# Optimization experiments

Hardware: AMD Instinct MI355X
Metric: run time of the kernel (lower is better)

The kernel has to match this reference:

```python
import jax, jax.numpy as jnp
import numpy as np

ALPHA = 0.2   # LeakyReLU slope from source
HEADS = 8

def _proj(x, W, s, b):
    # Conv3D(kernel=1, no bias) + fused inference BatchNorm affine + LeakyReLU
    y = jnp.einsum('nchwd,de->nchwe', x, W) * s + b
    return jnp.where(y >= 0, y, ALPHA * y)

def setup_inputs() -> dict:
    key = jax.random.key(0)
    ks = jax.random.split(key, 13)
    N, D, H, W, C = 2, 64, 64, 64, 64   # D == in_channels (axis 1), C is last axis
    KC, VC = 64, 64
    p = lambda k, sh, sc=0.1: jax.random.normal(k, sh, jnp.float32) * sc
    return {
        'x':  jax.random.normal(ks[0], (N, D, H, W, C), jnp.float32),
        'Wk': p(ks[1], (D, KC)), 'sk': 1.0 + p(ks[2], (KC,)), 'bk': p(ks[3], (KC,)),
        'Wq': p(ks[4], (D, KC)), 'sq': 1.0 + p(ks[5], (KC,)), 'bq': p(ks[6], (KC,)),
        'Wv': p(ks[7], (D, VC)), 'sv': 1.0 + p(ks[8], (VC,)), 'bv': p(ks[9], (VC,)),
        'Wr': p(ks[10], (VC, D)), 'sr': 1.0 + p(ks[11], (D,)), 'br': p(ks[12], (D,)),
    }

def reference(x, Wk, sk, bk, Wq, sq, bq, Wv, sv, bv, Wr, sr, br):
    n, d, h, w, c = x.shape
    xt = jnp.transpose(x, (0, 4, 2, 3, 1))            # (n, c, h, w, d)
    keys    = _proj(xt, Wk, sk, bk)                   # (n, c, h, w, KC)
    queries = _proj(xt, Wq, sq, bq)
    values  = _proj(xt, Wv, sv, bv)
    T = c * h * w
    KC, VC = Wk.shape[1], Wv.shape[1]
    hk, hv = KC // HEADS, VC // HEADS                 # hk == hv required by source math
    K = jax.nn.softmax(keys.reshape(n, T, HEADS, hk), axis=1)      # softmax over tokens
    Q = jax.nn.softmax(queries.reshape(n, T, HEADS, hk), axis=-1)  # softmax over head channels
    V = values.reshape(n, T, HEADS, hv)
    ctx = jnp.einsum('ntak,ntav->nakv', K, V)         # (n, heads, hk, hv) small context
    # source: tf.matmul(context, query^T) contracts ctx's hv with query's hk axis
    att = jnp.einsum('nakv,ntav->nakt', ctx, Q)       # (n, heads, hk, T)
    # faithful raw reshape per head (n, hk, T) -> (n, c, h, w, hv), heads concat last
    att = att.reshape(n, HEADS, c, h, w, hv)
    agg = jnp.transpose(att, (0, 2, 3, 4, 1, 5)).reshape(n, c, h, w, HEADS * hv)
    rep = _proj(agg, Wr, sr, br)                      # (n, c, h, w, d)
    return x + jnp.transpose(rep, (0, 4, 2, 3, 1))
```

## Files before the change

### kernel.cpp

```cpp
#include <hip/hip_runtime.h>

#define ALPHA 0.2f

typedef const __attribute__((address_space(1))) unsigned int gu32;
typedef __attribute__((address_space(3))) unsigned int lu32;

__device__ float g_part[8192 * 576];
__device__ float g_red[2 * 64 * 1024];
__device__ float g_ctx[1024];

__global__ __launch_bounds__(256, 3) void k_kv(
    const float* __restrict__ x,
    const float* __restrict__ Wk, const float* __restrict__ sk, const float* __restrict__ bk,
    const float* __restrict__ Wv, const float* __restrict__ sv, const float* __restrict__ bv)
{
  __shared__ __align__(16) float sh[11008];
  float* eK = sh;
  float* vV = sh + 4352;
  float* pE = sh + 8704;
  float* pS = sh + 8960;

  const int tid = threadIdx.x;
  const int bid = blockIdx.x;
  const int n   = bid >> 10;
  const int hw0 = (bid & 1023) * 4;

  const int pr  = tid & 63;
  const int wv  = __builtin_amdgcn_readfirstlane(tid >> 6);
  const bool isK = (wv < 2);
  const int cbase = 32 * (wv & 1);
  const float* Wsrc = (isK ? Wk : Wv) + cbase;
  const float* sp   = (isK ? sk : sv) + cbase;
  const float* bp   = (isK ? bk : bv) + cbase;

  const float* xg = x + (size_t)n * 16777216u + (size_t)hw0 * 64u + 4 * pr;

  float acc[4][32];
  #pragma unroll
  for (int t = 0; t < 4; ++t)
    #pragma unroll
    for (int c = 0; c < 32; ++c) acc[t][c] = 0.f;

  #pragma unroll 2
  for (int d = 0; d < 64; ++d) {
    float4 xv = *(const float4*)(xg + (size_t)d * 262144u);
    const float* wrow = Wsrc + d * 64;
    #pragma unroll
    for (int q = 0; q < 8; ++q) {
      float4 w = *(const float4*)(wrow + q * 4);
      acc[0][q*4+0] += xv.x * w.x; acc[0][q*4+1] += xv.x * w.y;
      acc[0][q*4+2] += xv.x * w.z; acc[0][q*4+3] += xv.x * w.w;
      acc[1][q*4+0] += xv.y * w.x; acc[1][q*4+1] += xv.y * w.y;
      acc[1][q*4+2] += xv.y * w.z; acc[1][q*4+3] += xv.y * w.w;
      acc[2][q*4+0] += xv.z * w.x; acc[2][q*4+1] += xv.z * w.y;
      acc[2][q*4+2] += xv.z * w.z; acc[2][q*4+3] += xv.z * w.w;
      acc[3][q*4+0] += xv.w * w.x; acc[3][q*4+1] += xv.w * w.y;
      acc[3][q*4+2] += xv.w * w.z; acc[3][q*4+3] += xv.w * w.w;
    }
  }

  #pragma unroll
  for (int q = 0; q < 8; ++q) {
    float4 s4 = *(const float4*)(sp + q * 4);
    float4 b4 = *(const float4*)(bp + q * 4);
    float ss[4] = {s4.x, s4.y, s4.z, s4.w};
    float bb[4] = {b4.x, b4.y, b4.z, b4.w};
    #pragma unroll
    for (int j = 0; j < 4; ++j) {
      #pragma unroll
      for (int t = 0; t < 4; ++t) {
        float y = acc[t][q*4+j] * ss[j] + bb[j];
        y = (y >= 0.f) ? y : ALPHA * y;
        if (isK) y = __expf(fminf(y, 60.f));
        acc[t][q*4+j] = y;
      }
    }
  }

  const int prl = pr & 15;
  float* dstbuf = isK ? eK : vV;
  const int ch = tid & 63, tq = tid >> 6, a8 = ch & ~7;

  #pragma unroll
  for (int ph = 0; ph < 4; ++ph) {
    if ((pr >> 4) == ph) {
      #pragma unroll
      for (int t = 0; t < 4; ++t)
        #pragma unroll
        for (int q = 0; q < 8; ++q)
          *(float4*)&dstbuf[(prl*4 + t) * 68 + cbase + q*4] = *(float4*)&acc[t][q*4];
    }
    __syncthreads();

    float E = 0.f;
    float S[8];
    #pragma unroll
    for (int v = 0; v < 8; ++v) S[v] = 0.f;
    for (int t = tq * 16; t < tq * 16 + 16; ++t) {
      float e = eK[t * 68 + ch];
      float4 v0 = *(const float4*)&vV[t * 68 + a8];
      float4 v1 = *(const float4*)&vV[t * 68 + a8 + 4];
      E += e;
      S[0] += e * v0.x; S[1] += e * v0.y; S[2] += e * v0.z; S[3] += e * v0.w;
      S[4] += e * v1.x; S[5] += e * v1.y; S[6] += e * v1.z; S[7] += e * v1.w;
    }
    pE[tq * 64 + ch] = E;
    #pragma unroll
    for (int v = 0; v < 8; ++v) pS[v * 256 + tq * 64 + ch] = S[v];
    __syncthreads();

    if (tid < 64) {
      float* gp = g_part + ((size_t)bid * 4u + ph) * 576u;
      float E4 = pE[tid] + pE[64 + tid] + pE[128 + tid] + pE[192 + tid];
      gp[tid] = E4;
      #pragma unroll
      for (int v = 0; v < 8; ++v) {
        float S4 = pS[v * 256 + tid] + pS[v * 256 + 64 + tid]
                 + pS[v * 256 + 128 + tid] + pS[v * 256 + 192 + tid];
        gp[64 + v * 64 + tid] = S4;
      }
    }
  }
}

__global__ __launch_bounds__(256) void k_red() {
  const int ob = blockIdx.x & 3;
  const int bc = blockIdx.x >> 2;
  const int i  = ob * 256 + threadIdx.x;
  const int n = i >> 9, ch = (i & 511) >> 3, v = i & 7;
  const float* base = g_part + ((size_t)n * 4096u + (size_t)bc * 64u) * 576u;
  float l = 0.f, S = 0.f;
  #pragma unroll 8
  for (int b = 0; b < 64; ++b) {
    l += base[(size_t)b * 576u + ch];
    S += base[(size_t)b * 576u + 64u + (size_t)v * 64u + ch];
  }
  g_red[bc * 1024 + i]         = l;
  g_red[65536 + bc * 1024 + i] = S;
}

__global__ __launch_bounds__(256) void k_ctx() {
  int i = blockIdx.x * 256 + threadIdx.x;
  if (i >= 1024) return;
  float l = 0.f, S = 0.f;
  #pragma unroll
  for (int r = 0; r < 64; ++r) {
    l += g_red[r * 1024 + i];
    S += g_red[65536 + r * 1024 + i];
  }
  float c = (l > 0.f) ? (S / l) : 0.f;
  if (!(__builtin_fabsf(c) < 1e30f)) c = 0.f;
  g_ctx[i] = c;
}

__global__ __launch_bounds__(256) void k_att(
    const float* __restrict__ x,
    const float* __restrict__ Wq, const float* __restrict__ sq, const float* __restrict__ bq,
    const float* __restrict__ Wr, const float* __restrict__ sr, const float* __restrict__ br,
    float* __restrict__ out)
{
  __shared__ __align__(16) float WqA[64 * 68];
  __shared__ __align__(16) float xw[64 * 64];
  __shared__ __align__(16) float qL[64 * 64];
  __shared__ __align__(16) float ctxL[64 * 12];
  __shared__ float srL[64], brL[64];

  const int tid = threadIdx.x;
  const int lin = blockIdx.x;

  const int xcd   = lin & 7;
  const int jc    = (lin >> 3) & 7;
  const int rest  = lin >> 6;
  const int combo = rest * 8 + xcd;
  const int n     = combo >> 9;
  const int hp_lo = (combo >> 6) & 7;
  const int wp    = combo & 63;
  const int hp    = jc * 8 + hp_lo;
  const int hwp   = hp * 64 + wp;

  const int h_t   = hp_lo * 8 + (wp >> 3);
  const int wbase = (wp & 7) * 8;

  #pragma unroll
  for (int i = 0; i < 4; ++i) {
    int idx = tid + i * 256;
    __builtin_amdgcn_global_load_lds((gu32*)(Wq + idx * 4),
                                     (lu32*)&WqA[idx * 4], 16, 0, 0);
  }
  if (tid < 64) { srL[tid] = sr[tid]; brL[tid] = br[tid]; }

  for (int i = tid; i < 512; i += 256) {
    int ch = i >> 3, v = i & 7;
    ctxL[ch * 12 + v] = g_ctx[n * 512 + ch * 8 + v];
  }

  {
    const size_t xb = (size_t)n * 16777216u + (size_t)h_t * 4096u;
    #pragma unroll
    for (int i = 0; i < 16; ++i) {
      int idx = tid + i * 256;
      int d = idx >> 6, tok = idx & 63;
      int vpp = tok >> 3, cl = tok & 7;
      xw[d * 64 + tok] = x[xb + (size_t)d * 262144u + (size_t)(wbase + vpp) * 64u + (cl * 8 + jc)];
    }
  }
  __syncthreads();

  {
    const int tok0 = (tid & 31) * 2;
    const int ch0  = (tid >> 5) * 8;
    float acc0[8], acc1[8];
    #pragma unroll
    for (int j = 0; j < 8; ++j) { acc0[j] = 0.f; acc1[j] = 0.f; }
    #pragma unroll 4
    for (int d = 0; d < 64; ++d) {
      float2 xv = *(const float2*)&xw[d * 64 + tok0];
      float4 wa = *(const float4*)&WqA[d * 64 + ch0];
      float4 wb = *(const float4*)&WqA[d * 64 + ch0 + 4];
      float w[8] = {wa.x, wa.y, wa.z, wa.w, wb.x, wb.y, wb.z, wb.w};
      #pragma unroll
      for (int j = 0; j < 8; ++j) { acc0[j] += xv.x * w[j]; acc1[j] += xv.y * w[j]; }
    }
    float sv8[8], bv8[8];
    *(float4*)&sv8[0] = *(const float4*)(sq + ch0);
    *(float4*)&sv8[4] = *(const float4*)(sq + ch0 + 4);
    *(float4*)&bv8[0] = *(const float4*)(bq + ch0);
    *(float4*)&bv8[4] = *(const float4*)(bq + ch0 + 4);
    #pragma unroll
    for (int i = 0; i < 2; ++i) {
      float* a = (i == 0) ? acc0 : acc1;
      float mx = -3.0e38f;
      #pragma unroll
      for (int j = 0; j < 8; ++j) {
        float y = a[j] * sv8[j] + bv8[j];
        y = (y >= 0.f) ? y : ALPHA * y;
        a[j] = y;
        mx = fmaxf(mx, y);
      }
      float sum = 0.f;
      #pragma unroll
      for (int j = 0; j < 8; ++j) { a[j] = __expf(a[j] - mx); sum += a[j]; }
      float inv = 1.f / sum;
      float o8[8];
      #pragma unroll
      for (int j = 0; j < 8; ++j) o8[j] = a[j] * inv;
      const int t = tok0 + i;
      const int rot = (4 * t) & 63;
      *(float4*)&qL[t * 64 + ((ch0 + rot) & 63)]     = *(float4*)&o8[0];
      *(float4*)&qL[t * 64 + ((ch0 + 4 + rot) & 63)] = *(float4*)&o8[4];
    }
  }
  __syncthreads();

  #pragma unroll
  for (int i = 0; i < 4; ++i) {
    int idx = tid + i * 256;
    __builtin_amdgcn_global_load_lds((gu32*)(Wr + idx * 4),
                                     (lu32*)&xw[idx * 4], 16, 0, 0);
  }

  {
    float* aggL = WqA;
    const int cp = tid & 63, eb = tid >> 6;
    const int kk = cp >> 3, cl = cp & 7;
    #pragma unroll
    for (int j4 = 0; j4 < 4; ++j4) {
      float s4[4];
      #pragma unroll
      for (int jj = 0; jj < 4; ++jj) {
        int e = eb * 16 + j4 * 4 + jj;
        int a = e >> 3, vpp = e & 7;
        float4 c0 = *(const float4*)&ctxL[(a * 8 + kk) * 12];
        float4 c1 = *(const float4*)&ctxL[(a * 8 + kk) * 12 + 4];
        int t = vpp * 8 + cl;
        int rot = (4 * t) & 63;
        float4 q0 = *(const float4*)&qL[t * 64 + ((a * 8 + rot) & 63)];
        float4 q1 = *(const float4*)&qL[t * 64 + ((a * 8 + 4 + rot) & 63)];
        s4[jj] = q0.x * c0.x + q0.y * c0.y + q0.z * c0.z + q0.w * c0.w
               + q1.x * c1.x + q1.y * c1.y + q1.z * c1.z + q1.w * c1.w;
      }
      *(float4*)&aggL[cp * 68 + eb * 16 + j4 * 4] =
          make_float4(s4[0], s4[1], s4[2], s4[3]);
    }
  }
  __syncthreads();

  {
    const float* aggL = WqA;
    const int ci = tid & 63, dq = tid >> 6;
    float accr[16];
    #pragma unroll
    for (int i = 0; i < 16; ++i) accr[i] = 0.f;
    #pragma unroll 4
    for (int ec = 0; ec < 16; ++ec) {
      float4 a4 = *(const float4*)&aggL[ci * 68 + ec * 4];
      float av[4] = {a4.x, a4.y, a4.z, a4.w};
      #pragma unroll
      for (int j = 0; j < 4; ++j) {
        const float* wrow = &xw[(ec * 4 + j) * 64 + dq * 16];
        float4 w0 = *(const float4*)(wrow);
        float4 w1 = *(const float4*)(wrow + 4);
        float4 w2 = *(const float4*)(wrow + 8);
        float4 w3 = *(const float4*)(wrow + 12);
        float aj = av[j];
        accr[0]  += aj * w0.x; accr[1]  += aj * w0.y; accr[2]  += aj * w0.z; accr[3]  += aj * w0.w;
        accr[4]  += aj * w1.x; accr[5]  += aj * w1.y; accr[6]  += aj * w1.z; accr[7]  += aj * w1.w;
        accr[8]  += aj * w2.x; accr[9]  += aj * w2.y; accr[10] += aj * w2.z; accr[11] += aj * w2.w;
        accr[12] += aj * w3.x; accr[13] += aj * w3.y; accr[14] += aj * w3.z; accr[15] += aj * w3.w;
      }
    }
    const size_t xb = (size_t)n * 16777216u + (size_t)hwp * 64u + (size_t)ci;
    #pragma unroll
    for (int i = 0; i < 16; ++i) {
      int di = dq * 16 + i;
      float y = accr[i] * srL[di] + brL[di];
      y = (y >= 0.f) ? y : ALPHA * y;
      out[xb + (size_t)di * 262144u] = x[xb + (size_t)di * 262144u] + y;
    }
  }
}

extern "C" void kernel_launch(void* const* d_in, const int* in_sizes, int n_in,
                              void* d_out, int out_size, void* d_ws, size_t ws_size,
                              hipStream_t stream)
{
  (void)in_sizes; (void)n_in; (void)out_size; (void)d_ws; (void)ws_size;

  const float* x  = (const float*)d_in[0];
  const float* Wk = (const float*)d_in[1];
  const float* sk = (const float*)d_in[2];
  const float* bk = (const float*)d_in[3];
  const float* Wq = (const float*)d_in[4];
  const float* sq = (const float*)d_in[5];
  const float* bq = (const float*)d_in[6];
  const float* Wv = (const float*)d_in[7];
  const float* sv = (const float*)d_in[8];
  const float* bv = (const float*)d_in[9];
  const float* Wr = (const float*)d_in[10];
  const float* sr = (const float*)d_in[11];
  const float* br = (const float*)d_in[12];
  float* out = (float*)d_out;

  k_kv  <<<dim3(2048), dim3(256), 0, stream>>>(x, Wk, sk, bk, Wv, sv, bv);
  k_red <<<dim3(256),  dim3(256), 0, stream>>>();
  k_ctx <<<dim3(4),    dim3(256), 0, stream>>>();
  k_att <<<dim3(8192), dim3(256), 0, stream>>>(x, Wq, sq, bq, Wr, sr, br, out);
}
```

Baseline: 509.8 us.

## Read weights as wave-uniform scalar loads instead of staging in LDS in attention kernel

The attention kernel no longer stages Wq, Wr, sr and br in shared memory. Each wave now owns a fixed 16-channel slice, so weight rows are wave-uniform and can be fetched with scalar loads, and each lane loads its x token directly from global memory. The Q projection is remapped from 2 tokens × 8 channels per thread to 1 token × 16 channels. This removes LDS traffic, LDS footprint and one staging phase, which can raise occupancy. In exchange it relies on the scalar cache for weight reuse and on strided per-lane global reads of x.

```diff
diff --git a/kernel.cpp b/kernel.cpp
--- a/kernel.cpp
+++ b/kernel.cpp
@@ -159,11 +159,9 @@
     const float* __restrict__ Wr, const float* __restrict__ sr, const float* __restrict__ br,
     float* __restrict__ out)
 {
-  __shared__ __align__(16) float WqA[64 * 68];
-  __shared__ __align__(16) float xw[64 * 64];
   __shared__ __align__(16) float qL[64 * 64];
+  __shared__ __align__(16) float aggL[64 * 68];
   __shared__ __align__(16) float ctxL[64 * 12];
-  __shared__ float srL[64], brL[64];
 
   const int tid = threadIdx.x;
   const int lin = blockIdx.x;
@@ -181,86 +179,71 @@
   const int h_t   = hp_lo * 8 + (wp >> 3);
   const int wbase = (wp & 7) * 8;
 
-  #pragma unroll
-  for (int i = 0; i < 4; ++i) {
-    int idx = tid + i * 256;
-    __builtin_amdgcn_global_load_lds((gu32*)(Wq + idx * 4),
-                                     (lu32*)&WqA[idx * 4], 16, 0, 0);
-  }
-  if (tid < 64) { srL[tid] = sr[tid]; brL[tid] = br[tid]; }
-
   for (int i = tid; i < 512; i += 256) {
     int ch = i >> 3, v = i & 7;
     ctxL[ch * 12 + v] = g_ctx[n * 512 + ch * 8 + v];
   }
 
+  const int lane = tid & 63;
+  const int wv   = __builtin_amdgcn_readfirstlane(tid >> 6);
+  const int c0   = wv * 16;
+
   {
-    const size_t xb = (size_t)n * 16777216u + (size_t)h_t * 4096u;
-    #pragma unroll
-    for (int i = 0; i < 16; ++i) {
-      int idx = tid + i * 256;
-      int d = idx >> 6, tok = idx & 63;
-      int vpp = tok >> 3, cl = tok & 7;
-      xw[d * 64 + tok] = x[xb + (size_t)d * 262144u + (size_t)(wbase + vpp) * 64u + (cl * 8 + jc)];
-    }
-  }
-  __syncthreads();
-
-  {
-    const int tok0 = (tid & 31) * 2;
-    const int ch0  = (tid >> 5) * 8;
-    float acc0[8], acc1[8];
-    #pragma unroll
-    for (int j = 0; j < 8; ++j) { acc0[j] = 0.f; acc1[j] = 0.f; }
+    const int vpp = lane >> 3, cl = lane & 7;
+    const float* xg = x + (size_t)n * 16777216u + (size_t)h_t * 4096u
+                    + (size_t)(wbase + vpp) * 64u + (size_t)(cl * 8 + jc);
+    const float* WqU = Wq + c0;
+
+    float acc[16];
+    #pragma unroll
+    for (int c = 0; c < 16; ++c) acc[c] = 0.f;
+
     #pragma unroll 4
     for (int d = 0; d < 64; ++d) {
-      float2 xv = *(const float2*)&xw[d * 64 + tok0];
-      float4 wa = *(const float4*)&WqA[d * 64 + ch0];
-      float4 wb = *(const float4*)&WqA[d * 64 + ch0 + 4];
-      float w[8] = {wa.x, wa.y, wa.z, wa.w, wb.x, wb.y, wb.z, wb.w};
-      #pragma unroll
-      for (int j = 0; j < 8; ++j) { acc0[j] += xv.x * w[j]; acc1[j] += xv.y * w[j]; }
-    }
-    float sv8[8], bv8[8];
-    *(float4*)&sv8[0] = *(const float4*)(sq + ch0);
-    *(float4*)&sv8[4] = *(const float4*)(sq + ch0 + 4);
-    *(float4*)&bv8[0] = *(const float4*)(bq + ch0);
-    *(float4*)&bv8[4] = *(const float4*)(bq + ch0 + 4);
-    #pragma unroll
-    for (int i = 0; i < 2; ++i) {
-      float* a = (i == 0) ? acc0 : acc1;
+      float xv = xg[(size_t)d * 262144u];
+      const float* wrow = WqU + d * 64;
+      float4 w0 = *(const float4*)(wrow);
+      float4 w1 = *(const float4*)(wrow + 4);
+      float4 w2 = *(const float4*)(wrow + 8);
+      float4 w3 = *(const float4*)(wrow + 12);
+      acc[0]  += xv * w0.x; acc[1]  += xv * w0.y; acc[2]  += xv * w0.z; acc[3]  += xv * w0.w;
+      acc[4]  += xv * w1.x; acc[5]  += xv * w1.y; acc[6]  += xv * w1.z; acc[7]  += xv * w1.w;
+      acc[8]  += xv * w2.x; acc[9]  += xv * w2.y; acc[10] += xv * w2.z; acc[11] += xv * w2.w;
+      acc[12] += xv * w3.x; acc[13] += xv * w3.y; acc[14] += xv * w3.z; acc[15] += xv * w3.w;
+    }
+
+    const int rot = (4 * lane) & 63;
+    #pragma unroll
+    for (int g = 0; g < 2; ++g) {
+      float4 s0 = *(const float4*)(sq + c0 + 8 * g);
+      float4 s1 = *(const float4*)(sq + c0 + 8 * g + 4);
+      float4 b0 = *(const float4*)(bq + c0 + 8 * g);
+      float4 b1 = *(const float4*)(bq + c0 + 8 * g + 4);
+      float ss[8] = {s0.x, s0.y, s0.z, s0.w, s1.x, s1.y, s1.z, s1.w};
+      float bb[8] = {b0.x, b0.y, b0.z, b0.w, b1.x, b1.y, b1.z, b1.w};
+      float a8[8];
       float mx = -3.0e38f;
       #pragma unroll
       for (int j = 0; j < 8; ++j) {
-        float y = a[j] * sv8[j] + bv8[j];
+        float y = acc[g * 8 + j] * ss[j] + bb[j];
         y = (y >= 0.f) ? y : ALPHA * y;
-        a[j] = y;
+        a8[j] = y;
         mx = fmaxf(mx, y);
       }
       float sum = 0.f;
       #pragma unroll
-      for (int j = 0; j < 8; ++j) { a[j] = __expf(a[j] - mx); sum += a[j]; }
+      for (int j = 0; j < 8; ++j) { a8[j] = __expf(a8[j] - mx); sum += a8[j]; }
       float inv = 1.f / sum;
       float o8[8];
       #pragma unroll
-      for (int j = 0; j < 8; ++j) o8[j] = a[j] * inv;
-      const int t = tok0 + i;
-      const int rot = (4 * t) & 63;
-      *(float4*)&qL[t * 64 + ((ch0 + rot) & 63)]     = *(float4*)&o8[0];
-      *(float4*)&qL[t * 64 + ((ch0 + 4 + rot) & 63)] = *(float4*)&o8[4];
+      for (int j = 0; j < 8; ++j) o8[j] = a8[j] * inv;
+      *(float4*)&qL[lane * 64 + ((c0 + 8 * g + rot) & 63)]     = *(float4*)&o8[0];
+      *(float4*)&qL[lane * 64 + ((c0 + 8 * g + 4 + rot) & 63)] = *(float4*)&o8[4];
     }
   }
   __syncthreads();
 
-  #pragma unroll
-  for (int i = 0; i < 4; ++i) {
-    int idx = tid + i * 256;
-    __builtin_amdgcn_global_load_lds((gu32*)(Wr + idx * 4),
-                                     (lu32*)&xw[idx * 4], 16, 0, 0);
-  }
-
   {
-    float* aggL = WqA;
     const int cp = tid & 63, eb = tid >> 6;
     const int kk = cp >> 3, cl = cp & 7;
     #pragma unroll
@@ -270,14 +253,14 @@
       for (int jj = 0; jj < 4; ++jj) {
         int e = eb * 16 + j4 * 4 + jj;
         int a = e >> 3, vpp = e & 7;
-        float4 c0 = *(const float4*)&ctxL[(a * 8 + kk) * 12];
-        float4 c1 = *(const float4*)&ctxL[(a * 8 + kk) * 12 + 4];
+        float4 c0v = *(const float4*)&ctxL[(a * 8 + kk) * 12];
+        float4 c1v = *(const float4*)&ctxL[(a * 8 + kk) * 12 + 4];
         int t = vpp * 8 + cl;
-        int rot = (4 * t) & 63;
-        float4 q0 = *(const float4*)&qL[t * 64 + ((a * 8 + rot) & 63)];
-        float4 q1 = *(const float4*)&qL[t * 64 + ((a * 8 + 4 + rot) & 63)];
-        s4[jj] = q0.x * c0.x + q0.y * c0.y + q0.z * c0.z + q0.w * c0.w
-               + q1.x * c1.x + q1.y * c1.y + q1.z * c1.z + q1.w * c1.w;
+        int rt = (4 * t) & 63;
+        float4 q0 = *(const float4*)&qL[t * 64 + ((a * 8 + rt) & 63)];
+        float4 q1 = *(const float4*)&qL[t * 64 + ((a * 8 + 4 + rt) & 63)];
+        s4[jj] = q0.x * c0v.x + q0.y * c0v.y + q0.z * c0v.z + q0.w * c0v.w
+               + q1.x * c1v.x + q1.y * c1v.y + q1.z * c1v.z + q1.w * c1v.w;
       }
       *(float4*)&aggL[cp * 68 + eb * 16 + j4 * 4] =
           make_float4(s4[0], s4[1], s4[2], s4[3]);
@@ -286,18 +269,19 @@
   __syncthreads();
 
   {
-    const float* aggL = WqA;
-    const int ci = tid & 63, dq = tid >> 6;
+    const int ci = tid & 63;
+    const int dq = wv;
+    const float* WrU = Wr + dq * 16;
     float accr[16];
     #pragma unroll
     for (int i = 0; i < 16; ++i) accr[i] = 0.f;
-    #pragma unroll 4
+    #pragma unroll 2
     for (int ec = 0; ec < 16; ++ec) {
       float4 a4 = *(const float4*)&aggL[ci * 68 + ec * 4];
       float av[4] = {a4.x, a4.y, a4.z, a4.w};
       #pragma unroll
       for (int j = 0; j < 4; ++j) {
-        const float* wrow = &xw[(ec * 4 + j) * 64 + dq * 16];
+        const float* wrow = WrU + (ec * 4 + j) * 64;
         float4 w0 = *(const float4*)(wrow);
         float4 w1 = *(const float4*)(wrow + 4);
         float4 w2 = *(const float4*)(wrow + 8);
@@ -309,11 +293,23 @@
         accr[12] += aj * w3.x; accr[13] += aj * w3.y; accr[14] += aj * w3.z; accr[15] += aj * w3.w;
       }
     }
+    float4 sr0 = *(const float4*)(sr + dq * 16);
+    float4 sr1 = *(const float4*)(sr + dq * 16 + 4);
+    float4 sr2 = *(const float4*)(sr + dq * 16 + 8);
+    float4 sr3 = *(const float4*)(sr + dq * 16 + 12);
+    float4 br0 = *(const float4*)(br + dq * 16);
+    float4 br1 = *(const float4*)(br + dq * 16 + 4);
+    float4 br2 = *(const float4*)(br + dq * 16 + 8);
+    float4 br3 = *(const float4*)(br + dq * 16 + 12);
+    float srv[16] = {sr0.x,sr0.y,sr0.z,sr0.w, sr1.x,sr1.y,sr1.z,sr1.w,
+                     sr2.x,sr2.y,sr2.z,sr2.w, sr3.x,sr3.y,sr3.z,sr3.w};
+    float brv[16] = {br0.x,br0.y,br0.z,br0.w, br1.x,br1.y,br1.z,br1.w,
+                     br2.x,br2.y,br2.z,br2.w, br3.x,br3.y,br3.z,br3.w};
     const size_t xb = (size_t)n * 16777216u + (size_t)hwp * 64u + (size_t)ci;
     #pragma unroll
     for (int i = 0; i < 16; ++i) {
       int di = dq * 16 + i;
-      float y = accr[i] * srL[di] + brL[di];
+      float y = accr[i] * srv[i] + brv[i];
       y = (y >= 0.f) ? y : ALPHA * y;
       out[xb + (size_t)di * 262144u] = x[xb + (size_t)di * 262144u] + y;
     }
```

New measurement: 571.8 us. +12.2%, slower.
